# Kernel tuning notes

Measured on AMD Instinct MI355X. Metric: run time of the kernel, lower is better.

The kernel has to match this reference:

```python
import jax, jax.numpy as jnp
import numpy as np

N_NODES = 500000
N_EDGES = 16000000
N_PAIRS = 100000


def setup_inputs() -> dict:
    key = jax.random.key(0)
    k1, k2, k3, k4, k5 = jax.random.split(key, 5)
    x = jax.random.normal(k1, (N_NODES, 1), dtype=jnp.float32)
    node_weight = jax.random.uniform(k2, (N_NODES, 1), dtype=jnp.float32)
    bias = jnp.zeros((1,), dtype=jnp.float32)  # GCNConv bias, zero-init
    edge_index = jax.random.randint(k3, (2, N_EDGES), 0, N_NODES, dtype=jnp.int64)
    home = jax.random.randint(k4, (N_PAIRS,), 0, N_NODES, dtype=jnp.int64)
    away = jax.random.randint(k5, (N_PAIRS,), 0, N_NODES, dtype=jnp.int64)
    return {"x": x, "node_weight": node_weight, "bias": bias,
            "edge_index": edge_index, "home": home, "away": away}


def reference(x, node_weight, bias, edge_index, home, away):
    # GCNConv(1,1), add_self_loops=False, edge_weight = ones, weight = 1.
    N = x.shape[0]
    row, col = edge_index[0], edge_index[1]  # row = source j, col = target i
    ones = jnp.ones(row.shape[0], dtype=x.dtype)
    # symmetric normalization: deg computed at target (col) with unit weights
    deg = jax.ops.segment_sum(ones, col, num_segments=N)
    deg_inv_sqrt = jnp.where(deg > 0, jax.lax.rsqrt(jnp.where(deg > 0, deg, 1.0)), 0.0)
    norm = deg_inv_sqrt[row] * deg_inv_sqrt[col]          # [E]
    msg = norm * x[row, 0]                                # gather + scale, [E]
    agg = jax.ops.segment_sum(msg, col, num_segments=N)   # scatter-add, [N]
    conv_out = agg[:, None] + bias                        # [N,1]
    # data.x = sigmoid(data.x * node_weight + conv_out)
    x_new = jax.nn.sigmoid(x * node_weight + conv_out)    # [N,1]
    out = x_new[home] - x_new[away]                       # [B,1]
    return jnp.sign(out)
```

## Files before the change

### kernel.cpp

```cpp
#include <hip/hip_runtime.h>


#define NPB_SHIFT 11
#define NPB       2048
#define NBMAX     256
#define GB        1024
#define TEDGE     256
#define TBIN      1024
#define VEC       2
#define TBKT      1024
#define CAP       32
#define CAPP      33


__device__ __forceinline__ unsigned wave_incl_scan(unsigned v) {
    #pragma unroll
    for (int d = 1; d < 64; d <<= 1) {
        unsigned n = __shfl_up((int)v, d, 64);
        if ((threadIdx.x & 63) >= (unsigned)d) v += n;
    }
    return v;
}

__device__ __forceinline__ unsigned block_excl_scan256(unsigned v, unsigned* lds,
                                                       unsigned* total) {
    int lane = threadIdx.x & 63, w = threadIdx.x >> 6;
    unsigned incl = wave_incl_scan(v);
    if (lane == 63) lds[w] = incl;
    __syncthreads();
    if (threadIdx.x == 0) {
        unsigned run = 0;
        #pragma unroll
        for (int i = 0; i < 4; ++i) { unsigned t = lds[i]; lds[i] = run; run += t; }
        lds[4] = run;
    }
    __syncthreads();
    unsigned e = incl - v + lds[w];
    *total = lds[4];
    __syncthreads();
    return e;
}


__global__ __launch_bounds__(TEDGE) void k_hist(const int* __restrict__ col,
                                                unsigned* __restrict__ counts,
                                                int E, int cpb, int NB) {
    __shared__ unsigned hist[NBMAX];
    for (int b = threadIdx.x; b < NBMAX; b += TEDGE) hist[b] = 0;
    __syncthreads();
    int start = blockIdx.x * cpb;
    int end = min(E, start + cpb);
    int e = start + threadIdx.x * 4;
    for (; e + 3 < end; e += TEDGE * 4) {
        int4 c = *(const int4*)(col + e);
        atomicAdd(&hist[(unsigned)c.x >> NPB_SHIFT], 1u);
        atomicAdd(&hist[(unsigned)c.y >> NPB_SHIFT], 1u);
        atomicAdd(&hist[(unsigned)c.z >> NPB_SHIFT], 1u);
        atomicAdd(&hist[(unsigned)c.w >> NPB_SHIFT], 1u);
    }
    #pragma unroll
    for (int k = 0; k < 4; ++k)
        if (e + k < end) atomicAdd(&hist[(unsigned)col[e + k] >> NPB_SHIFT], 1u);
    __syncthreads();
    for (int b = threadIdx.x; b < NB; b += TEDGE)
        counts[(size_t)b * GB + blockIdx.x] = hist[b];
}

__global__ __launch_bounds__(256) void k_scanA(unsigned* __restrict__ counts,
                                               unsigned* __restrict__ rowsum) {
    __shared__ unsigned lds[8];
    unsigned carry = 0;
    #pragma unroll
    for (int ch = 0; ch < GB / 256; ++ch) {
        size_t idx = (size_t)blockIdx.x * GB + ch * 256 + threadIdx.x;
        unsigned v = counts[idx];
        unsigned tot;
        unsigned e = block_excl_scan256(v, lds, &tot);
        counts[idx] = e + carry;
        carry += tot;
    }
    if (threadIdx.x == 0) rowsum[blockIdx.x] = carry;
}

__global__ __launch_bounds__(256) void k_scanB(const unsigned* __restrict__ rowsum,
                                               unsigned* __restrict__ rowbase, int NB) {
    __shared__ unsigned lds[8];
    unsigned v = (threadIdx.x < (unsigned)NB) ? rowsum[threadIdx.x] : 0u;
    unsigned tot;
    unsigned e = block_excl_scan256(v, lds, &tot);
    if (threadIdx.x < (unsigned)NB) rowbase[threadIdx.x] = e;
}

__global__ __launch_bounds__(TBIN) void k_bin(const int* __restrict__ row,
                                              const int* __restrict__ col,
                                              const unsigned* __restrict__ counts,
                                              const unsigned* __restrict__ rowbase,
                                              unsigned* __restrict__ packed,
                                              int E, int cpb, int NB) {
    __shared__ unsigned stage[NBMAX * CAPP];
    __shared__ unsigned gbase[NBMAX];
    __shared__ unsigned scnt[NBMAX];
    __shared__ unsigned flushed[NBMAX];

    for (int b = threadIdx.x; b < NB; b += TBIN) {
        gbase[b] = counts[(size_t)b * GB + blockIdx.x] + rowbase[b];
        scnt[b] = 0; flushed[b] = 0;
    }
    __syncthreads();

    int start = blockIdx.x * cpb;
    int end = min(E, start + cpb);
    int wv = threadIdx.x >> 6, lane = threadIdx.x & 63;
    const int RB = TBIN * VEC;

#define PROC(cc, rr) {                                                        \
        unsigned b_ = (unsigned)(cc) >> NPB_SHIFT;                            \
        unsigned v_ = ((unsigned)(rr) << NPB_SHIFT) | ((unsigned)(cc) & (NPB - 1u)); \
        unsigned pos_ = atomicAdd(&scnt[b_], 1u);                             \
        if (pos_ - flushed[b_] < CAP)                                         \
            stage[b_ * CAPP + (pos_ & (CAP - 1u))] = v_;                      \
        else                                                                  \
            packed[gbase[b_] + pos_] = v_; }

    for (int base = start; base < end; base += RB) {
        int e = base + threadIdx.x * VEC;
        if (e + VEC - 1 < end) {
            int2 c2 = *(const int2*)(col + e);
            int2 r2 = *(const int2*)(row + e);
            PROC(c2.x, r2.x);
            PROC(c2.y, r2.y);
        } else {
            #pragma unroll
            for (int k = 0; k < VEC; ++k)
                if (e + k < end) { PROC(col[e + k], row[e + k]); }
        }
        __syncthreads();
        for (int b = wv; b < NB; b += TBIN / 64) {
            unsigned f = flushed[b], s = scnt[b];
            unsigned pend = s - f;
            unsigned n = (pend >= CAP) ? CAP : (pend & ~15u);
            if (n) {
                unsigned gb = gbase[b];
                if (lane < n)
                    packed[gb + f + lane] = stage[b * CAPP + ((f + lane) & (CAP - 1))];
                if (lane == 0) flushed[b] = (pend >= CAP) ? s : (f + n);
            }
        }
        __syncthreads();
    }
    for (int b = wv; b < NB; b += TBIN / 64) {
        unsigned f = flushed[b], s = scnt[b];
        if (f + lane < s)
            packed[gbase[b] + f + lane] = stage[b * CAPP + ((f + lane) & (CAP - 1))];
    }
#undef PROC
}

__global__ __launch_bounds__(TBKT) void k_degdis(const unsigned* __restrict__ packed,
                                                 const unsigned* __restrict__ rowbase,
                                                 const float* __restrict__ x,
                                                 float* __restrict__ dis,
                                                 float* __restrict__ px,
                                                 int E, int N, int NB) {
    __shared__ unsigned cnt[NPB];
    for (int j = threadIdx.x; j < NPB; j += TBKT) cnt[j] = 0;
    __syncthreads();
    int b = blockIdx.x;
    unsigned base = rowbase[b];
    unsigned end = (b == NB - 1) ? (unsigned)E : rowbase[b + 1];
    #pragma unroll 4
    for (unsigned e = base + threadIdx.x; e < end; e += TBKT)
        atomicAdd(&cnt[packed[e] & (NPB - 1u)], 1u);
    __syncthreads();
    int nbase = b << NPB_SHIFT;
    for (int j = threadIdx.x; j < NPB; j += TBKT) {
        int i = nbase + j;
        if (i < N) {
            unsigned d = cnt[j];
            float v = d ? rsqrtf((float)d) : 0.0f;
            dis[i] = v;
            px[i] = v * x[i];
        }
    }
}

__global__ __launch_bounds__(TBKT) void k_scatter_z(
        const unsigned* __restrict__ packed, const float* __restrict__ px,
        const unsigned* __restrict__ rowbase, const float* __restrict__ x,
        const float* __restrict__ nw, const float* __restrict__ dis,
        const float* __restrict__ bias, float* __restrict__ z,
        int E, int N, int NB) {
    __shared__ float acc[NPB];
    for (int j = threadIdx.x; j < NPB; j += TBKT) acc[j] = 0.0f;
    __syncthreads();
    int b = blockIdx.x;
    unsigned base = rowbase[b];
    unsigned end = (b == NB - 1) ? (unsigned)E : rowbase[b + 1];
    #pragma unroll 4
    for (unsigned e = base + threadIdx.x; e < end; e += TBKT) {
        unsigned v = packed[e];
        atomicAdd(&acc[v & (NPB - 1u)], px[v >> NPB_SHIFT]);
    }
    __syncthreads();
    int nbase = b << NPB_SHIFT;
    float b0 = bias[0];
    for (int j = threadIdx.x; j < NPB; j += TBKT) {
        int i = nbase + j;
        if (i < N) z[i] = fmaf(x[i], nw[i], fmaf(dis[i], acc[j], b0));
    }
}

__global__ void k_pairs(const float* __restrict__ z, const int* __restrict__ home,
                        const int* __restrict__ away, float* __restrict__ out, int n) {
    int i = blockIdx.x * blockDim.x + threadIdx.x;
    if (i < n) {
        float d = z[home[i]] - z[away[i]];
        out[i] = (d > 0.0f) ? 1.0f : ((d < 0.0f) ? -1.0f : 0.0f);
    }
}


__global__ void f_degree(const int* __restrict__ col, int* __restrict__ deg, int e4) {
    int i = blockIdx.x * blockDim.x + threadIdx.x;
    int stride = gridDim.x * blockDim.x;
    const int4* c4 = (const int4*)col;
    for (; i < e4; i += stride) {
        int4 c = c4[i];
        atomicAdd(&deg[c.x], 1); atomicAdd(&deg[c.y], 1);
        atomicAdd(&deg[c.z], 1); atomicAdd(&deg[c.w], 1);
    }
}
__global__ void f_dis(unsigned* __restrict__ degdis, const float* __restrict__ x,
                      float* __restrict__ px, int n) {
    int i = blockIdx.x * blockDim.x + threadIdx.x;
    int stride = gridDim.x * blockDim.x;
    float* disf = (float*)degdis;
    for (; i < n; i += stride) {
        unsigned d = degdis[i];
        float v = (d > 0u) ? rsqrtf((float)d) : 0.0f;
        disf[i] = v;
        px[i] = v * x[i];
    }
}
__global__ void f_scatter(const int* __restrict__ row, const int* __restrict__ col,
                          const float* __restrict__ px, float* __restrict__ agg, int e4) {
    int i = blockIdx.x * blockDim.x + threadIdx.x;
    int stride = gridDim.x * blockDim.x;
    const int4* r4 = (const int4*)row;
    const int4* c4 = (const int4*)col;
    for (; i < e4; i += stride) {
        int4 r = r4[i];
        int4 c = c4[i];
        atomicAdd(&agg[c.x], px[r.x]); atomicAdd(&agg[c.y], px[r.y]);
        atomicAdd(&agg[c.z], px[r.z]); atomicAdd(&agg[c.w], px[r.w]);
    }
}
__global__ void f_z(const float* __restrict__ x, const float* __restrict__ nw,
                    const float* __restrict__ dis, const float* __restrict__ bias,
                    float* __restrict__ agg, int n) {
    int i = blockIdx.x * blockDim.x + threadIdx.x;
    int stride = gridDim.x * blockDim.x;
    float b = bias[0];
    for (; i < n; i += stride)
        agg[i] = fmaf(x[i], nw[i], fmaf(dis[i], agg[i], b));
}


extern "C" void kernel_launch(void* const* d_in, const int* in_sizes, int n_in,
                              void* d_out, int out_size, void* d_ws, size_t ws_size,
                              hipStream_t stream) {
    const float* x    = (const float*)d_in[0];
    const float* nw   = (const float*)d_in[1];
    const float* bias = (const float*)d_in[2];
    const int*   ei   = (const int*)d_in[3];
    const int*   home = (const int*)d_in[4];
    const int*   away = (const int*)d_in[5];
    float* out = (float*)d_out;

    const int N = in_sizes[0];
    const int E = in_sizes[3] / 2;
    const int P = in_sizes[4];

    const int* row = ei;
    const int* col = ei + E;

    const int NB  = (N + NPB - 1) >> NPB_SHIFT;
    const int cpb = (((E + GB - 1) / GB) + 3) & ~3;

    auto align256 = [](size_t v) { return (v + 255) & ~(size_t)255; };
    size_t off = 0;
    size_t o_counts = off; off += align256((size_t)NBMAX * GB * 4);
    size_t o_rowsum = off; off += align256(NBMAX * 4);
    size_t o_rowbas = off; off += align256(NBMAX * 4);
    size_t o_dis    = off; off += align256((size_t)N * 4);
    size_t o_px     = off; off += align256((size_t)N * 4);
    size_t o_z      = off; off += align256((size_t)N * 4);
    size_t o_pack   = off; off += align256((size_t)E * 4);
    size_t need = off;

    bool fast = (NB <= NBMAX) && ((size_t)N <= (1u << (32 - NPB_SHIFT)))
                && (ws_size >= need);

    if (fast) {
        char* base = (char*)d_ws;
        unsigned* counts  = (unsigned*)(base + o_counts);
        unsigned* rowsum  = (unsigned*)(base + o_rowsum);
        unsigned* rowbase = (unsigned*)(base + o_rowbas);
        float*    dis     = (float*)(base + o_dis);
        float*    px      = (float*)(base + o_px);
        float*    z       = (float*)(base + o_z);
        unsigned* packed  = (unsigned*)(base + o_pack);

        k_hist<<<GB, TEDGE, 0, stream>>>(col, counts, E, cpb, NB);
        k_scanA<<<NB, 256, 0, stream>>>(counts, rowsum);
        k_scanB<<<1, 256, 0, stream>>>(rowsum, rowbase, NB);
        k_bin<<<GB, TBIN, 0, stream>>>(row, col, counts, rowbase, packed, E, cpb, NB);
        k_degdis<<<NB, TBKT, 0, stream>>>(packed, rowbase, x, dis, px, E, N, NB);
        k_scatter_z<<<NB, TBKT, 0, stream>>>(packed, px, rowbase, x, nw, dis, bias,
                                             z, E, N, NB);
        k_pairs<<<(P + 255) / 256, 256, 0, stream>>>(z, home, away, out, P);
    } else {
        size_t slot = align256((size_t)N * 4);
        int*   deg = (int*)d_ws;
        float* agg = (float*)((char*)d_ws + slot);
        float* px  = (float*)((char*)d_ws + 2 * slot);
        const int e4 = E / 4;
        hipMemsetAsync(d_ws, 0, 2 * slot, stream);
        f_degree<<<2048, 256, 0, stream>>>(col, deg, e4);
        f_dis<<<2048, 256, 0, stream>>>((unsigned*)deg, x, px, N);
        f_scatter<<<2048, 256, 0, stream>>>(row, col, px, agg, e4);
        f_z<<<2048, 256, 0, stream>>>(x, nw, (const float*)deg, bias, agg, N);
        k_pairs<<<(P + 255) / 256, 256, 0, stream>>>(agg, home, away, out, P);
    }
}
```

Baseline: 390.0 us.

## Split per-bucket degree and scatter kernels into slices with partial merges

The degree-count and scatter-add kernels, each launched with one block per 2048-node bucket (about 245 blocks), are split into 8 slice blocks per bucket. Each slice accumulates into its own LDS histogram and writes a partial array to global memory, and two new small merge kernels sum the 8 partials to produce dis/px and z. This is meant to raise parallelism and fill more CUs than one block per bucket allows. In exchange it adds two kernel launches and extra global traffic for the partial arrays, which are 8 times N words.

```diff
diff --git a/kernel.cpp b/kernel.cpp
--- a/kernel.cpp
+++ b/kernel.cpp
@@ -8,7 +8,9 @@
 #define TEDGE     256
 #define TBIN      1024
 #define VEC       2
-#define TBKT      1024
+#define TSL       512
+#define SSPLIT    8
+#define TMERGE    1024
 #define CAP       32
 #define CAPP      33
 
@@ -156,27 +158,42 @@
 #undef PROC
 }
 
-__global__ __launch_bounds__(TBKT) void k_degdis(const unsigned* __restrict__ packed,
-                                                 const unsigned* __restrict__ rowbase,
-                                                 const float* __restrict__ x,
-                                                 float* __restrict__ dis,
-                                                 float* __restrict__ px,
-                                                 int E, int N, int NB) {
+__global__ __launch_bounds__(TSL) void k_deg_slice(const unsigned* __restrict__ packed,
+                                                   const unsigned* __restrict__ rowbase,
+                                                   unsigned* __restrict__ pcnt,
+                                                   int E, int NB) {
     __shared__ unsigned cnt[NPB];
-    for (int j = threadIdx.x; j < NPB; j += TBKT) cnt[j] = 0;
-    __syncthreads();
-    int b = blockIdx.x;
+    for (int j = threadIdx.x; j < NPB; j += TSL) cnt[j] = 0;
+    __syncthreads();
+    int b = blockIdx.x / SSPLIT, s = blockIdx.x % SSPLIT;
     unsigned base = rowbase[b];
     unsigned end = (b == NB - 1) ? (unsigned)E : rowbase[b + 1];
+    unsigned len = end - base;
+    unsigned sl = (len + SSPLIT - 1) / SSPLIT;
+    unsigned sb = base + s * sl;
+    unsigned se = min(end, sb + sl);
     #pragma unroll 4
-    for (unsigned e = base + threadIdx.x; e < end; e += TBKT)
+    for (unsigned e = sb + threadIdx.x; e < se; e += TSL)
         atomicAdd(&cnt[packed[e] & (NPB - 1u)], 1u);
     __syncthreads();
+    unsigned* dst = pcnt + (size_t)blockIdx.x * NPB;
+    for (int j = threadIdx.x; j < NPB; j += TSL) dst[j] = cnt[j];
+}
+
+__global__ __launch_bounds__(TMERGE) void k_dis(const unsigned* __restrict__ pcnt,
+                                                const float* __restrict__ x,
+                                                float* __restrict__ dis,
+                                                float* __restrict__ px,
+                                                int N, int NB) {
+    int b = blockIdx.x;
+    const unsigned* src = pcnt + (size_t)b * SSPLIT * NPB;
     int nbase = b << NPB_SHIFT;
-    for (int j = threadIdx.x; j < NPB; j += TBKT) {
+    for (int j = threadIdx.x; j < NPB; j += TMERGE) {
         int i = nbase + j;
         if (i < N) {
-            unsigned d = cnt[j];
+            unsigned d = 0;
+            #pragma unroll
+            for (int s = 0; s < SSPLIT; ++s) d += src[s * NPB + j];
             float v = d ? rsqrtf((float)d) : 0.0f;
             dis[i] = v;
             px[i] = v * x[i];
@@ -184,29 +201,48 @@
     }
 }
 
-__global__ __launch_bounds__(TBKT) void k_scatter_z(
+__global__ __launch_bounds__(TSL) void k_scatter_slice(
         const unsigned* __restrict__ packed, const float* __restrict__ px,
-        const unsigned* __restrict__ rowbase, const float* __restrict__ x,
-        const float* __restrict__ nw, const float* __restrict__ dis,
-        const float* __restrict__ bias, float* __restrict__ z,
-        int E, int N, int NB) {
+        const unsigned* __restrict__ rowbase, float* __restrict__ pacc,
+        int E, int NB) {
     __shared__ float acc[NPB];
-    for (int j = threadIdx.x; j < NPB; j += TBKT) acc[j] = 0.0f;
-    __syncthreads();
-    int b = blockIdx.x;
+    for (int j = threadIdx.x; j < NPB; j += TSL) acc[j] = 0.0f;
+    __syncthreads();
+    int b = blockIdx.x / SSPLIT, s = blockIdx.x % SSPLIT;
     unsigned base = rowbase[b];
     unsigned end = (b == NB - 1) ? (unsigned)E : rowbase[b + 1];
+    unsigned len = end - base;
+    unsigned sl = (len + SSPLIT - 1) / SSPLIT;
+    unsigned sb = base + s * sl;
+    unsigned se = min(end, sb + sl);
     #pragma unroll 4
-    for (unsigned e = base + threadIdx.x; e < end; e += TBKT) {
+    for (unsigned e = sb + threadIdx.x; e < se; e += TSL) {
         unsigned v = packed[e];
         atomicAdd(&acc[v & (NPB - 1u)], px[v >> NPB_SHIFT]);
     }
     __syncthreads();
+    float* dst = pacc + (size_t)blockIdx.x * NPB;
+    for (int j = threadIdx.x; j < NPB; j += TSL) dst[j] = acc[j];
+}
+
+__global__ __launch_bounds__(TMERGE) void k_z(const float* __restrict__ pacc,
+                                              const float* __restrict__ x,
+                                              const float* __restrict__ nw,
+                                              const float* __restrict__ dis,
+                                              const float* __restrict__ bias,
+                                              float* __restrict__ z, int N, int NB) {
+    int b = blockIdx.x;
+    const float* src = pacc + (size_t)b * SSPLIT * NPB;
     int nbase = b << NPB_SHIFT;
     float b0 = bias[0];
-    for (int j = threadIdx.x; j < NPB; j += TBKT) {
+    for (int j = threadIdx.x; j < NPB; j += TMERGE) {
         int i = nbase + j;
-        if (i < N) z[i] = fmaf(x[i], nw[i], fmaf(dis[i], acc[j], b0));
+        if (i < N) {
+            float a = 0.0f;
+            #pragma unroll
+            for (int s = 0; s < SSPLIT; ++s) a += src[s * NPB + j];
+            z[i] = fmaf(x[i], nw[i], fmaf(dis[i], a, b0));
+        }
     }
 }
 
@@ -295,6 +331,7 @@
     size_t o_dis    = off; off += align256((size_t)N * 4);
     size_t o_px     = off; off += align256((size_t)N * 4);
     size_t o_z      = off; off += align256((size_t)N * 4);
+    size_t o_part   = off; off += align256((size_t)NB * SSPLIT * NPB * 4);
     size_t o_pack   = off; off += align256((size_t)E * 4);
     size_t need = off;
 
@@ -309,15 +346,18 @@
         float*    dis     = (float*)(base + o_dis);
         float*    px      = (float*)(base + o_px);
         float*    z       = (float*)(base + o_z);
+        unsigned* part    = (unsigned*)(base + o_part);
         unsigned* packed  = (unsigned*)(base + o_pack);
 
         k_hist<<<GB, TEDGE, 0, stream>>>(col, counts, E, cpb, NB);
         k_scanA<<<NB, 256, 0, stream>>>(counts, rowsum);
         k_scanB<<<1, 256, 0, stream>>>(rowsum, rowbase, NB);
         k_bin<<<GB, TBIN, 0, stream>>>(row, col, counts, rowbase, packed, E, cpb, NB);
-        k_degdis<<<NB, TBKT, 0, stream>>>(packed, rowbase, x, dis, px, E, N, NB);
-        k_scatter_z<<<NB, TBKT, 0, stream>>>(packed, px, rowbase, x, nw, dis, bias,
-                                             z, E, N, NB);
+        k_deg_slice<<<NB * SSPLIT, TSL, 0, stream>>>(packed, rowbase, part, E, NB);
+        k_dis<<<NB, TMERGE, 0, stream>>>(part, x, dis, px, N, NB);
+        k_scatter_slice<<<NB * SSPLIT, TSL, 0, stream>>>(packed, px, rowbase,
+                                                         (float*)part, E, NB);
+        k_z<<<NB, TMERGE, 0, stream>>>((const float*)part, x, nw, dis, bias, z, N, NB);
         k_pairs<<<(P + 255) / 256, 256, 0, stream>>>(z, home, away, out, P);
     } else {
         size_t slot = align256((size_t)N * 4);
```

After: 386.3 us. No clear change (-1.0%).
